# Performance work log

Measured on AMD Instinct MI355X. Metric: run time of the kernel, lower is better.

The kernel has to match this reference:

```python
import jax, jax.numpy as jnp
import numpy as np

B, Tq, Tk, D, H = 8, 128, 512, 256, 256

def setup_inputs() -> dict:
    key = jax.random.key(0)
    k1, k2, k3, k4, k5, k6, k7 = jax.random.split(key, 7)
    scale = 1.0 / np.sqrt(D)
    return {
        "queries": jax.random.normal(k1, (B, Tq, D), dtype=jnp.float32),
        "keys": jax.random.normal(k2, (B, Tk, D), dtype=jnp.float32),
        "values": jax.random.normal(k3, (B, Tk, D), dtype=jnp.float32),
        "valid_lens": jax.random.randint(k4, (B,), 1, Tk + 1),
        "Wq": jax.random.normal(k5, (D, H), dtype=jnp.float32) * scale,
        "Wk": jax.random.normal(k6, (D, H), dtype=jnp.float32) * scale,
        "wv": jax.random.normal(k7, (H,), dtype=jnp.float32) * (1.0 / np.sqrt(H)),
    }

def masked_softmax(scores, valid_lens):
    # scores: (B, Tq, Tk); valid_lens: (B,)
    T = scores.shape[-1]
    mask = jnp.arange(T) < valid_lens[:, None, None]  # (B,1,Tk) -> broadcast
    neg_inf = jnp.finfo(scores.dtype).min
    probs = jax.nn.softmax(jnp.where(mask, scores, neg_inf), axis=-1)
    fully_masked = ~jnp.any(mask, axis=-1, keepdims=True)
    return jnp.where(fully_masked, jnp.zeros_like(probs), probs)

def reference(queries, keys, values, valid_lens, Wq, Wk, wv):
    q_proj = jnp.einsum('bqd,dh->bqh', queries, Wq)  # (B,Tq,H)
    k_proj = jnp.einsum('bkd,dh->bkh', keys, Wk)      # (B,Tk,H)
    features = jnp.tanh(q_proj[:, :, None, :] + k_proj[:, None, :, :])  # (B,Tq,Tk,H)
    scores = jnp.einsum('bqkh,h->bqk', features, wv)  # (B,Tq,Tk)
    attn = masked_softmax(scores, valid_lens)
    # dropout is identity at p=0.0 / eval
    return jnp.einsum('bqk,bkd->bqd', attn, values)
```

## Files before the change

### kernel.cpp

```cpp
#include <hip/hip_runtime.h>
#include <hip/hip_bf16.h>

#define B_  8
#define TQ_ 128
#define TK_ 512
#define D_  256
#define H_  256

#define KSCALE 2.8853900817779268f

__device__ __forceinline__ float fast_exp2(float x) {
    return __builtin_amdgcn_exp2f(x);
}

__device__ __forceinline__ float wave_red_min(float v) {
#pragma unroll
    for (int o = 32; o > 0; o >>= 1) v = fminf(v, __shfl_xor(v, o));
    return v;
}
__device__ __forceinline__ float wave_red_sum(float v) {
#pragma unroll
    for (int o = 32; o > 0; o >>= 1) v += __shfl_xor(v, o);
    return v;
}

__global__ __launch_bounds__(512) void proj_kernel(
    const float* __restrict__ queries, const float* __restrict__ keys,
    const float* __restrict__ Wq, const float* __restrict__ Wk,
    float* __restrict__ qp, float* __restrict__ kpT)
{
    __shared__ __align__(16) float xs[8 * 256];
    __shared__ float tile[8 * 258];

    const int t  = threadIdx.x;
    const int h  = t & 255;
    const int rh = t >> 8;
    const bool isQ = (blockIdx.x < 128);
    const float* X; const float* W; int b, r0;
    if (isQ) {
        b = blockIdx.x >> 4; r0 = (blockIdx.x & 15) * 8;
        X = queries + ((size_t)b * TQ_ + r0) * D_;  W = Wq;
    } else {
        int id = blockIdx.x - 128;
        b = id >> 6; r0 = (id & 63) * 8;
        X = keys + ((size_t)b * TK_ + r0) * D_;     W = Wk;
    }

#pragma unroll
    for (int i = 0; i < 4; ++i) {
        int e = i * 512 + t;
        xs[e] = X[e];
    }
    __syncthreads();

    const float* Wcol = W + h;
    float w0[4], w1[4], w2[4];
#pragma unroll
    for (int j = 0; j < 4; ++j) w0[j] = Wcol[(size_t)j * H_];
#pragma unroll
    for (int j = 0; j < 4; ++j) w1[j] = Wcol[(size_t)(4 + j) * H_];

    float acc[4];
#pragma unroll
    for (int r = 0; r < 4; ++r) acc[r] = 0.0f;
    const int r0l = rh * 4;

    for (int d = 0; d < D_; d += 4) {
        const int dn = (d + 8) & (D_ - 1);
#pragma unroll
        for (int j = 0; j < 4; ++j) w2[j] = Wcol[(size_t)(dn + j) * H_];
#pragma unroll
        for (int r = 0; r < 4; ++r) {
            const float4 x4 = *reinterpret_cast<const float4*>(&xs[(r0l + r) * 256 + d]);
            acc[r] = fmaf(x4.x, w0[0], acc[r]);
            acc[r] = fmaf(x4.y, w0[1], acc[r]);
            acc[r] = fmaf(x4.z, w0[2], acc[r]);
            acc[r] = fmaf(x4.w, w0[3], acc[r]);
        }
#pragma unroll
        for (int j = 0; j < 4; ++j) { w0[j] = w1[j]; w1[j] = w2[j]; }
    }
#pragma unroll
    for (int r = 0; r < 4; ++r) acc[r] *= KSCALE;

    if (isQ) {
        float* dst = qp + ((size_t)b * TQ_ + r0 + r0l) * H_ + h;
#pragma unroll
        for (int r = 0; r < 4; ++r) dst[(size_t)r * H_] = acc[r];
    } else {
#pragma unroll
        for (int r = 0; r < 4; ++r) tile[(r0l + r) * 258 + h] = acc[r];
        __syncthreads();
        const int rp = t & 7, h0 = t >> 3;
        float* dst = kpT + (size_t)b * (H_ * TK_) + r0 + rp;
#pragma unroll
        for (int i = 0; i < 4; ++i) {
            int hr = h0 + i * 64;
            dst[(size_t)hr * TK_] = tile[rp * 258 + hr];
        }
    }
}

__global__ __launch_bounds__(512) void attn_kernel(
    const float* __restrict__ qp, const float* __restrict__ kpT,
    const float* __restrict__ values, const int* __restrict__ valid_lens,
    const float* __restrict__ wv, float* __restrict__ out)
{
    __shared__ __align__(16) float qw[H_];
    __shared__ __align__(16) float wvs[H_];
    __shared__ float pe[TK_];
    __shared__ float red[8];
    __shared__ float red2[8];
    __shared__ float acch[256];

    const int t = threadIdx.x;
    const int b = blockIdx.y;
    const int q = blockIdx.x;

    const int len = valid_lens[b];

    const float* qpb = qp + ((size_t)b * TQ_ + q) * H_;
    if (t < 256) qw[t] = qpb[t];
    else         wvs[t - 256] = wv[t - 256];
    __syncthreads();

    const int k = t;
    const float* kcol = kpT + (size_t)b * (H_ * TK_) + k;
    float a = 0.f;
    const float4* qw4 = reinterpret_cast<const float4*>(qw);
    const float4* wv4 = reinterpret_cast<const float4*>(wvs);
#pragma unroll 2
    for (int h4 = 0; h4 < 64; ++h4) {
        float k0 = kcol[(size_t)(h4 * 4 + 0) * TK_];
        float k1 = kcol[(size_t)(h4 * 4 + 1) * TK_];
        float k2 = kcol[(size_t)(h4 * 4 + 2) * TK_];
        float k3 = kcol[(size_t)(h4 * 4 + 3) * TK_];
        const float4 q4 = qw4[h4];
        const float4 w4 = wv4[h4];
        float e0 = fast_exp2(q4.x + k0);
        float e1 = fast_exp2(q4.y + k1);
        float e2 = fast_exp2(q4.z + k2);
        float e3 = fast_exp2(q4.w + k3);
        a = fmaf(w4.x, __builtin_amdgcn_rcpf(1.0f + e0), a);
        a = fmaf(w4.y, __builtin_amdgcn_rcpf(1.0f + e1), a);
        a = fmaf(w4.z, __builtin_amdgcn_rcpf(1.0f + e2), a);
        a = fmaf(w4.w, __builtin_amdgcn_rcpf(1.0f + e3), a);
    }

    const int lane = t & 63, wid = t >> 6;
    const bool valid = (k < len);
    const float BIG = 3.0e38f;

    float m = wave_red_min(valid ? a : BIG);
    if (lane == 0) red[wid] = m;
    __syncthreads();
    float mrow = fminf(fminf(fminf(red[0], red[1]), fminf(red[2], red[3])),
                       fminf(fminf(red[4], red[5]), fminf(red[6], red[7])));

    float e = valid ? fast_exp2((mrow - a) * KSCALE) : 0.f;
    pe[k] = e;
    float S = wave_red_sum(e);
    if (lane == 0) red2[wid] = S;
    __syncthreads();
    float rs = 1.0f / (((red2[0] + red2[1]) + (red2[2] + red2[3])) +
                       ((red2[4] + red2[5]) + (red2[6] + red2[7])));

    const int d = t & 255;
    const int half = t >> 8;
    float c = 0.f;
    const float* vb = values + (size_t)b * (TK_ * D_) + (size_t)(half * 256) * D_ + d;
    const float* pb = &pe[half * 256];
#pragma unroll 8
    for (int kk = 0; kk < 256; ++kk) {
        c = fmaf(pb[kk], vb[(size_t)kk * D_], c);
    }
    if (half == 1) acch[d] = c;
    __syncthreads();
    if (half == 0) {
        out[((size_t)b * TQ_ + q) * D_ + d] = (c + acch[d]) * rs;
    }
}

extern "C" void kernel_launch(void* const* d_in, const int* in_sizes, int n_in,
                              void* d_out, int out_size, void* d_ws, size_t ws_size,
                              hipStream_t stream) {
    const float* queries    = (const float*)d_in[0];
    const float* keys       = (const float*)d_in[1];
    const float* values     = (const float*)d_in[2];
    const int*   valid_lens = (const int*)  d_in[3];
    const float* Wq         = (const float*)d_in[4];
    const float* Wk         = (const float*)d_in[5];
    const float* wv         = (const float*)d_in[6];
    float* out = (float*)d_out;

    float* qp  = (float*)d_ws;
    float* kpT = qp + (size_t)B_ * TQ_ * H_;

    proj_kernel<<<640, 512, 0, stream>>>(queries, keys, Wq, Wk, qp, kpT);
    attn_kernel<<<dim3(TQ_, B_), 512, 0, stream>>>(qp, kpT, values, valid_lens, wv, out);
}
```

Before: 135.0 us.

## Process two queries per attention block and retile projection kernel

```diff
diff --git a/kernel.cpp b/kernel.cpp
--- a/kernel.cpp
+++ b/kernel.cpp
@@ -13,6 +13,13 @@
     return __builtin_amdgcn_exp2f(x);
 }
 
+__device__ __forceinline__ float fast_rcp(float y) {
+    float r = __int_as_float(0x7EF311C3 - __float_as_int(y));
+    r = r * fmaf(-y, r, 2.0f);
+    r = r * fmaf(-y, r, 2.0f);
+    return r;
+}
+
 __device__ __forceinline__ float wave_red_min(float v) {
 #pragma unroll
     for (int o = 32; o > 0; o >>= 1) v = fminf(v, __shfl_xor(v, o));
@@ -29,75 +36,77 @@
     const float* __restrict__ Wq, const float* __restrict__ Wk,
     float* __restrict__ qp, float* __restrict__ kpT)
 {
-    __shared__ __align__(16) float xs[8 * 256];
-    __shared__ float tile[8 * 258];
-
-    const int t  = threadIdx.x;
-    const int h  = t & 255;
-    const int rh = t >> 8;
-    const bool isQ = (blockIdx.x < 128);
+    __shared__ __align__(16) float4 xs4[16 * 64];
+    __shared__ __align__(16) float tile[16 * 260];
+
+    const int t = threadIdx.x;
+    const bool isQ = (blockIdx.x < 64);
     const float* X; const float* W; int b, r0;
     if (isQ) {
-        b = blockIdx.x >> 4; r0 = (blockIdx.x & 15) * 8;
+        b = blockIdx.x >> 3; r0 = (blockIdx.x & 7) * 16;
         X = queries + ((size_t)b * TQ_ + r0) * D_;  W = Wq;
     } else {
-        int id = blockIdx.x - 128;
-        b = id >> 6; r0 = (id & 63) * 8;
+        int id = blockIdx.x - 64;
+        b = id >> 5; r0 = (id & 31) * 16;
         X = keys + ((size_t)b * TK_ + r0) * D_;     W = Wk;
     }
 
-#pragma unroll
-    for (int i = 0; i < 4; ++i) {
-        int e = i * 512 + t;
-        xs[e] = X[e];
-    }
-    __syncthreads();
-
-    const float* Wcol = W + h;
-    float w0[4], w1[4], w2[4];
-#pragma unroll
-    for (int j = 0; j < 4; ++j) w0[j] = Wcol[(size_t)j * H_];
-#pragma unroll
-    for (int j = 0; j < 4; ++j) w1[j] = Wcol[(size_t)(4 + j) * H_];
-
-    float acc[4];
-#pragma unroll
-    for (int r = 0; r < 4; ++r) acc[r] = 0.0f;
-    const int r0l = rh * 4;
-
-    for (int d = 0; d < D_; d += 4) {
-        const int dn = (d + 8) & (D_ - 1);
-#pragma unroll
-        for (int j = 0; j < 4; ++j) w2[j] = Wcol[(size_t)(dn + j) * H_];
-#pragma unroll
-        for (int r = 0; r < 4; ++r) {
-            const float4 x4 = *reinterpret_cast<const float4*>(&xs[(r0l + r) * 256 + d]);
-            acc[r] = fmaf(x4.x, w0[0], acc[r]);
-            acc[r] = fmaf(x4.y, w0[1], acc[r]);
-            acc[r] = fmaf(x4.z, w0[2], acc[r]);
-            acc[r] = fmaf(x4.w, w0[3], acc[r]);
-        }
-#pragma unroll
-        for (int j = 0; j < 4; ++j) { w0[j] = w1[j]; w1[j] = w2[j]; }
-    }
-#pragma unroll
-    for (int r = 0; r < 4; ++r) acc[r] *= KSCALE;
+    const float4* X4 = reinterpret_cast<const float4*>(X);
+    xs4[t]       = X4[t];
+    xs4[t + 512] = X4[t + 512];
+    __syncthreads();
+
+    const int hq = t & 63;
+    const int rg = t >> 6;
+    const int rA = rg * 2, rB = rA + 1;
+    const float4* W4 = reinterpret_cast<const float4*>(W) + hq;
+
+    float4 a0 = make_float4(0.f, 0.f, 0.f, 0.f);
+    float4 a1 = make_float4(0.f, 0.f, 0.f, 0.f);
+
+#pragma unroll 4
+    for (int d4 = 0; d4 < 64; ++d4) {
+        const float4 xa = xs4[rA * 64 + d4];
+        const float4 xb = xs4[rB * 64 + d4];
+        const float4 w0 = W4[(size_t)(d4 * 4 + 0) * 64];
+        const float4 w1 = W4[(size_t)(d4 * 4 + 1) * 64];
+        const float4 w2 = W4[(size_t)(d4 * 4 + 2) * 64];
+        const float4 w3 = W4[(size_t)(d4 * 4 + 3) * 64];
+        a0.x = fmaf(w0.x, xa.x, a0.x); a0.y = fmaf(w0.y, xa.x, a0.y);
+        a0.z = fmaf(w0.z, xa.x, a0.z); a0.w = fmaf(w0.w, xa.x, a0.w);
+        a1.x = fmaf(w0.x, xb.x, a1.x); a1.y = fmaf(w0.y, xb.x, a1.y);
+        a1.z = fmaf(w0.z, xb.x, a1.z); a1.w = fmaf(w0.w, xb.x, a1.w);
+        a0.x = fmaf(w1.x, xa.y, a0.x); a0.y = fmaf(w1.y, xa.y, a0.y);
+        a0.z = fmaf(w1.z, xa.y, a0.z); a0.w = fmaf(w1.w, xa.y, a0.w);
+        a1.x = fmaf(w1.x, xb.y, a1.x); a1.y = fmaf(w1.y, xb.y, a1.y);
+        a1.z = fmaf(w1.z, xb.y, a1.z); a1.w = fmaf(w1.w, xb.y, a1.w);
+        a0.x = fmaf(w2.x, xa.z, a0.x); a0.y = fmaf(w2.y, xa.z, a0.y);
+        a0.z = fmaf(w2.z, xa.z, a0.z); a0.w = fmaf(w2.w, xa.z, a0.w);
+        a1.x = fmaf(w2.x, xb.z, a1.x); a1.y = fmaf(w2.y, xb.z, a1.y);
+        a1.z = fmaf(w2.z, xb.z, a1.z); a1.w = fmaf(w2.w, xb.z, a1.w);
+        a0.x = fmaf(w3.x, xa.w, a0.x); a0.y = fmaf(w3.y, xa.w, a0.y);
+        a0.z = fmaf(w3.z, xa.w, a0.z); a0.w = fmaf(w3.w, xa.w, a0.w);
+        a1.x = fmaf(w3.x, xb.w, a1.x); a1.y = fmaf(w3.y, xb.w, a1.y);
+        a1.z = fmaf(w3.z, xb.w, a1.z); a1.w = fmaf(w3.w, xb.w, a1.w);
+    }
+    a0.x *= KSCALE; a0.y *= KSCALE; a0.z *= KSCALE; a0.w *= KSCALE;
+    a1.x *= KSCALE; a1.y *= KSCALE; a1.z *= KSCALE; a1.w *= KSCALE;
 
     if (isQ) {
-        float* dst = qp + ((size_t)b * TQ_ + r0 + r0l) * H_ + h;
-#pragma unroll
-        for (int r = 0; r < 4; ++r) dst[(size_t)r * H_] = acc[r];
+        float* dst = qp + ((size_t)b * TQ_ + r0) * H_ + hq * 4;
+        *reinterpret_cast<float4*>(dst + (size_t)rA * H_) = a0;
+        *reinterpret_cast<float4*>(dst + (size_t)rB * H_) = a1;
     } else {
-#pragma unroll
-        for (int r = 0; r < 4; ++r) tile[(r0l + r) * 258 + h] = acc[r];
+        *reinterpret_cast<float4*>(&tile[rA * 260 + hq * 4]) = a0;
+        *reinterpret_cast<float4*>(&tile[rB * 260 + hq * 4]) = a1;
         __syncthreads();
-        const int rp = t & 7, h0 = t >> 3;
-        float* dst = kpT + (size_t)b * (H_ * TK_) + r0 + rp;
-#pragma unroll
-        for (int i = 0; i < 4; ++i) {
-            int hr = h0 + i * 64;
-            dst[(size_t)hr * TK_] = tile[rp * 258 + hr];
-        }
+        const int h = t >> 1, half = t & 1;
+        float v[8];
+#pragma unroll
+        for (int i = 0; i < 8; ++i) v[i] = tile[(half * 8 + i) * 260 + h];
+        float* dst = kpT + (size_t)b * (H_ * TK_) + (size_t)h * TK_ + r0 + half * 8;
+        *reinterpret_cast<float4*>(dst)     = make_float4(v[0], v[1], v[2], v[3]);
+        *reinterpret_cast<float4*>(dst + 4) = make_float4(v[4], v[5], v[6], v[7]);
     }
 }
 
@@ -106,78 +115,79 @@
     const float* __restrict__ values, const int* __restrict__ valid_lens,
     const float* __restrict__ wv, float* __restrict__ out)
 {
-    __shared__ __align__(16) float qw[H_];
+    __shared__ __align__(16) float2 qw[H_];
     __shared__ __align__(16) float wvs[H_];
-    __shared__ float pe[TK_];
-    __shared__ float red[8];
-    __shared__ float red2[8];
-    __shared__ float acch[256];
+    __shared__ __align__(16) float2 pe2[TK_];
+    __shared__ float redm[2][8], reds[2][8];
+    __shared__ float acch[2 * 256];
 
     const int t = threadIdx.x;
     const int b = blockIdx.y;
-    const int q = blockIdx.x;
+    const int q0 = blockIdx.x * 2;
 
     const int len = valid_lens[b];
 
-    const float* qpb = qp + ((size_t)b * TQ_ + q) * H_;
-    if (t < 256) qw[t] = qpb[t];
+    const float* qpb = qp + ((size_t)b * TQ_ + q0) * H_;
+    if (t < 256) qw[t] = make_float2(qpb[t], qpb[256 + t]);
     else         wvs[t - 256] = wv[t - 256];
     __syncthreads();
 
     const int k = t;
     const float* kcol = kpT + (size_t)b * (H_ * TK_) + k;
-    float a = 0.f;
-    const float4* qw4 = reinterpret_cast<const float4*>(qw);
-    const float4* wv4 = reinterpret_cast<const float4*>(wvs);
-#pragma unroll 2
-    for (int h4 = 0; h4 < 64; ++h4) {
-        float k0 = kcol[(size_t)(h4 * 4 + 0) * TK_];
-        float k1 = kcol[(size_t)(h4 * 4 + 1) * TK_];
-        float k2 = kcol[(size_t)(h4 * 4 + 2) * TK_];
-        float k3 = kcol[(size_t)(h4 * 4 + 3) * TK_];
-        const float4 q4 = qw4[h4];
-        const float4 w4 = wv4[h4];
-        float e0 = fast_exp2(q4.x + k0);
-        float e1 = fast_exp2(q4.y + k1);
-        float e2 = fast_exp2(q4.z + k2);
-        float e3 = fast_exp2(q4.w + k3);
-        a = fmaf(w4.x, __builtin_amdgcn_rcpf(1.0f + e0), a);
-        a = fmaf(w4.y, __builtin_amdgcn_rcpf(1.0f + e1), a);
-        a = fmaf(w4.z, __builtin_amdgcn_rcpf(1.0f + e2), a);
-        a = fmaf(w4.w, __builtin_amdgcn_rcpf(1.0f + e3), a);
+    float a0 = 0.f, a1 = 0.f;
+#pragma unroll 8
+    for (int h = 0; h < H_; ++h) {
+        const float kk = kcol[(size_t)h * TK_];
+        const float2 q2 = qw[h];
+        const float w = wvs[h];
+        const float e0 = fast_exp2(q2.x + kk);
+        const float e1 = fast_exp2(q2.y + kk);
+        a0 = fmaf(w, fast_rcp(1.0f + e0), a0);
+        a1 = fmaf(w, fast_rcp(1.0f + e1), a1);
     }
 
     const int lane = t & 63, wid = t >> 6;
     const bool valid = (k < len);
     const float BIG = 3.0e38f;
 
-    float m = wave_red_min(valid ? a : BIG);
-    if (lane == 0) red[wid] = m;
-    __syncthreads();
-    float mrow = fminf(fminf(fminf(red[0], red[1]), fminf(red[2], red[3])),
-                       fminf(fminf(red[4], red[5]), fminf(red[6], red[7])));
-
-    float e = valid ? fast_exp2((mrow - a) * KSCALE) : 0.f;
-    pe[k] = e;
-    float S = wave_red_sum(e);
-    if (lane == 0) red2[wid] = S;
-    __syncthreads();
-    float rs = 1.0f / (((red2[0] + red2[1]) + (red2[2] + red2[3])) +
-                       ((red2[4] + red2[5]) + (red2[6] + red2[7])));
+    float m0 = wave_red_min(valid ? a0 : BIG);
+    float m1 = wave_red_min(valid ? a1 : BIG);
+    if (lane == 0) { redm[0][wid] = m0; redm[1][wid] = m1; }
+    __syncthreads();
+    float mr0 = redm[0][0], mr1 = redm[1][0];
+#pragma unroll
+    for (int i = 1; i < 8; ++i) { mr0 = fminf(mr0, redm[0][i]); mr1 = fminf(mr1, redm[1][i]); }
+
+    const float e0 = valid ? fast_exp2((mr0 - a0) * KSCALE) : 0.f;
+    const float e1 = valid ? fast_exp2((mr1 - a1) * KSCALE) : 0.f;
+    pe2[k] = make_float2(e0, e1);
+    float S0 = wave_red_sum(e0);
+    float S1 = wave_red_sum(e1);
+    if (lane == 0) { reds[0][wid] = S0; reds[1][wid] = S1; }
+    __syncthreads();
+    float s0 = 0.f, s1 = 0.f;
+#pragma unroll
+    for (int i = 0; i < 8; ++i) { s0 += reds[0][i]; s1 += reds[1][i]; }
+    const float rs0 = 1.0f / s0, rs1 = 1.0f / s1;
 
     const int d = t & 255;
     const int half = t >> 8;
-    float c = 0.f;
+    float c0 = 0.f, c1 = 0.f;
     const float* vb = values + (size_t)b * (TK_ * D_) + (size_t)(half * 256) * D_ + d;
-    const float* pb = &pe[half * 256];
+    const float2* pb = &pe2[half * 256];
 #pragma unroll 8
     for (int kk = 0; kk < 256; ++kk) {
-        c = fmaf(pb[kk], vb[(size_t)kk * D_], c);
-    }
-    if (half == 1) acch[d] = c;
+        const float v = vb[(size_t)kk * D_];
+        const float2 p = pb[kk];
+        c0 = fmaf(p.x, v, c0);
+        c1 = fmaf(p.y, v, c1);
+    }
+    if (half == 1) { acch[d] = c0; acch[256 + d] = c1; }
     __syncthreads();
     if (half == 0) {
-        out[((size_t)b * TQ_ + q) * D_ + d] = (c + acch[d]) * rs;
+        float* ob = out + ((size_t)b * TQ_ + q0) * D_ + d;
+        ob[0]  = (c0 + acch[d])       * rs0;
+        ob[D_] = (c1 + acch[256 + d]) * rs1;
     }
 }
 
@@ -196,6 +206,6 @@
     float* qp  = (float*)d_ws;
     float* kpT = qp + (size_t)B_ * TQ_ * H_;
 
-    proj_kernel<<<640, 512, 0, stream>>>(queries, keys, Wq, Wk, qp, kpT);
-    attn_kernel<<<dim3(TQ_, B_), 512, 0, stream>>>(qp, kpT, values, valid_lens, wv, out);
-}
+    proj_kernel<<<320, 512, 0, stream>>>(queries, keys, Wq, Wk, qp, kpT);
+    attn_kernel<<<dim3(TQ_ / 2, B_), 512, 0, stream>>>(qp, kpT, values, valid_lens, wv, out);
+}
```

Result: slower. 145.9 us (+8.1%).
